# Kernel optimization log

Hardware: AMD Instinct MI355X
Metric: run time of the kernel (lower is better)

The kernel has to match this reference:

```python
import jax, jax.numpy as jnp
import numpy as np

N_NODES = 100000
N_EDGES = 1600000
D = 64          # embedding_dim (in_feats == out_feats)
H = 1           # num_heads
NEG_SLOPE = 0.2


def setup_inputs() -> dict:
    key = jax.random.key(0)
    k = jax.random.split(key, 7)
    feat = jax.random.normal(k[0], (N_NODES, D), dtype=jnp.float32)
    W = jax.random.normal(k[1], (D, H * D), dtype=jnp.float32) * (1.0 / np.sqrt(D))
    attn_l = jax.random.normal(k[2], (1, H, D), dtype=jnp.float32) * (1.0 / np.sqrt(D))
    attn_r = jax.random.normal(k[3], (1, H, D), dtype=jnp.float32) * (1.0 / np.sqrt(D))
    bias = jnp.zeros((H * D,), dtype=jnp.float32)
    src = jax.random.randint(k[4], (N_EDGES,), 0, N_NODES, dtype=jnp.int32)
    dst = jax.random.randint(k[5], (N_EDGES,), 0, N_NODES, dtype=jnp.int32)
    return {"feat": feat, "W": W, "attn_l": attn_l, "attn_r": attn_r,
            "bias": bias, "src": src, "dst": dst}


def reference(feat, W, attn_l, attn_r, bias, src, dst):
    # fc (no bias), view to [N, H, D_out]
    ft = (feat @ W).reshape(-1, H, D)                       # [N, H, D]
    # per-node attention halves
    el = jnp.sum(ft * attn_l, axis=-1, keepdims=True)       # [N, H, 1]
    er = jnp.sum(ft * attn_r, axis=-1, keepdims=True)       # [N, H, 1]
    # edge score: u_add_v then leaky_relu
    e = el[src] + er[dst]                                    # [E, H, 1]
    e = jnp.where(e > 0, e, NEG_SLOPE * e)
    # edge softmax over incoming edges of each destination node
    emax = jax.ops.segment_max(e, dst, num_segments=N_NODES)  # [N, H, 1]
    e_exp = jnp.exp(e - emax[dst])
    denom = jax.ops.segment_sum(e_exp, dst, num_segments=N_NODES)  # [N, H, 1]
    a = e_exp / denom[dst]                                   # [E, H, 1]
    # u_mul_e + sum aggregation to destination
    m = ft[src] * a                                          # [E, H, D]
    rst = jax.ops.segment_sum(m, dst, num_segments=N_NODES)  # [N, H, D]
    # residual (Identity since in_feats == out_feats) + bias
    rst = rst + feat.reshape(-1, H, D)
    rst = rst + bias.reshape(1, H, D)
    return rst
```

## Files before the change

kernel.cpp:

```cpp
#include <hip/hip_runtime.h>
#include <hip/hip_fp16.h>
#include <math.h>

#define NN 100000
#define NE 1600000
#define D 64
#define NEG_SLOPE 0.2f
#define NBKT 391
#define NBIN 391
#define CHUNKB 4096
#define BSLOT 5120
#define NTILE 1563

typedef __attribute__((ext_vector_type(8))) short short8;
typedef __attribute__((ext_vector_type(4))) float f32x4;

template<int CTRL>
__device__ __forceinline__ float dpp_add(float x) {
    int y = __builtin_amdgcn_update_dpp(0, __float_as_int(x), CTRL, 0xf, 0xf, true);
    return x + __int_as_float(y);
}
template<int CTRL>
__device__ __forceinline__ float dpp_max(float x) {
    int xi = __float_as_int(x);
    int y = __builtin_amdgcn_update_dpp(xi, xi, CTRL, 0xf, 0xf, false);
    return fmaxf(x, __int_as_float(y));
}
__device__ __forceinline__ float wave_sum63(float x) {
    x = dpp_add<0x111>(x); x = dpp_add<0x112>(x); x = dpp_add<0x114>(x);
    x = dpp_add<0x118>(x); x = dpp_add<0x142>(x); x = dpp_add<0x143>(x);
    return x;
}
__device__ __forceinline__ float wave_max63(float x) {
    x = dpp_max<0x111>(x); x = dpp_max<0x112>(x); x = dpp_max<0x114>(x);
    x = dpp_max<0x118>(x); x = dpp_max<0x142>(x); x = dpp_max<0x143>(x);
    return x;
}
__device__ __forceinline__ float rdlane_f(float v, int l) {
    return __int_as_float(__builtin_amdgcn_readlane(__float_as_int(v), l));
}
__device__ __forceinline__ unsigned bf16_1(float f) {
    unsigned x = __float_as_uint(f);
    return (x + 0x7fffu + ((x >> 16) & 1u)) >> 16;
}
__device__ __forceinline__ unsigned bfpack(float a, float b) {
    return bf16_1(a) | (bf16_1(b) << 16);
}

__global__ __launch_bounds__(256) void k_bin(const int* __restrict__ src,
                                             const int* __restrict__ dst,
                                             unsigned* __restrict__ bcnt,
                                             unsigned* __restrict__ binned) {
    __shared__ unsigned lh[NBKT];
    int t = threadIdx.x;
    unsigned b0 = blockIdx.x * CHUNKB;
    unsigned b1 = min(b0 + CHUNKB, (unsigned)NE);
    if (b0 >= b1) return;
    unsigned n4 = (b1 - b0) >> 2;
    for (int k = t; k < NBKT; k += 256) lh[k] = 0u;
    __syncthreads();
    const int4* d4 = (const int4*)(dst + b0);
    const int4* s4 = (const int4*)(src + b0);
    for (unsigned i = t; i < n4; i += 256) {
        int4 v = d4[i];
        atomicAdd(&lh[((unsigned)v.x) >> 8], 1u);
        atomicAdd(&lh[((unsigned)v.y) >> 8], 1u);
        atomicAdd(&lh[((unsigned)v.z) >> 8], 1u);
        atomicAdd(&lh[((unsigned)v.w) >> 8], 1u);
    }
    __syncthreads();
    for (int k = t; k < NBKT; k += 256) {
        unsigned c = lh[k];
        if (c) lh[k] = (unsigned)k * BSLOT + atomicAdd(&bcnt[k], c);
    }
    __syncthreads();
    for (unsigned i = t; i < n4; i += 256) {
        int4 dv = d4[i];
        int4 sv = s4[i];
        { unsigned d_=(unsigned)dv.x, s_=(unsigned)sv.x;
          unsigned pos=atomicAdd(&lh[d_>>8],1u); binned[pos]=(s_<<8)|(d_&255u); }
        { unsigned d_=(unsigned)dv.y, s_=(unsigned)sv.y;
          unsigned pos=atomicAdd(&lh[d_>>8],1u); binned[pos]=(s_<<8)|(d_&255u); }
        { unsigned d_=(unsigned)dv.z, s_=(unsigned)sv.z;
          unsigned pos=atomicAdd(&lh[d_>>8],1u); binned[pos]=(s_<<8)|(d_&255u); }
        { unsigned d_=(unsigned)dv.w, s_=(unsigned)sv.w;
          unsigned pos=atomicAdd(&lh[d_>>8],1u); binned[pos]=(s_<<8)|(d_&255u); }
    }
}

__global__ __launch_bounds__(256) void k_sg(
    const unsigned* __restrict__ bcnt, const unsigned* __restrict__ binned,
    int* __restrict__ perm, uint2* __restrict__ rowBE,
    const float* __restrict__ feat, const float* __restrict__ W,
    const float* __restrict__ attn_l, const float* __restrict__ attn_r,
    __half* __restrict__ ft, float* __restrict__ el, float* __restrict__ er)
{
    __shared__ __align__(16) char smem[22784];
    int t = threadIdx.x;

    if (blockIdx.x < NBKT) {
        unsigned* lh    = (unsigned*)smem;
        unsigned* cur   = (unsigned*)smem + 256;
        unsigned* stage = (unsigned*)smem + 512;
        int b = blockIdx.x;
        unsigned beg = (unsigned)b * BSLOT;
        unsigned cnt = min(bcnt[b], (unsigned)BSLOT);
        lh[t] = 0u;
        __syncthreads();
        for (unsigned i = t; i < cnt; i += 256) {
            unsigned w = binned[beg + i];
            stage[i] = w;
            atomicAdd(&lh[w & 255u], 1u);
        }
        __syncthreads();
        for (int off = 1; off < 256; off <<= 1) {
            unsigned u = (t >= off) ? lh[t - off] : 0u;
            __syncthreads();
            lh[t] += u;
            __syncthreads();
        }
        unsigned start = (t == 0) ? 0u : lh[t - 1];
        unsigned node = ((unsigned)b << 8) + (unsigned)t;
        if (node < NN) {
            uint2 be; be.x = beg + start; be.y = beg + lh[t];
            rowBE[node] = be;
        }
        cur[t] = start;
        __syncthreads();
        for (unsigned i = t; i < cnt; i += 256) {
            unsigned w = stage[i];
            unsigned pos = atomicAdd(&cur[w & 255u], 1u);
            perm[beg + pos] = (int)(w >> 8);
        }
        return;
    }

    unsigned short* Ab = (unsigned short*)smem;
    unsigned short* Bb = (unsigned short*)(smem + 8192);
    float* wlS = (float*)(smem + 16384);
    float* wrS = (float*)(smem + 16640);
    int n0 = (int)(blockIdx.x - NBKT) * 64;

    {
        int k = t >> 2, s = t & 3;
        float pl = 0.f, pr = 0.f;
        #pragma unroll
        for (int q = 0; q < 4; ++q) {
            int seg = s + q * 4;
            float4 f = *(const float4*)(W + k * 64 + seg * 4);
            float4 a = *(const float4*)(attn_l + seg * 4);
            float4 b = *(const float4*)(attn_r + seg * 4);
            pl += f.x*a.x + f.y*a.y + f.z*a.z + f.w*a.w;
            pr += f.x*b.x + f.y*b.y + f.z*b.z + f.w*b.w;
        }
        pl += __shfl_xor(pl, 1, 64); pl += __shfl_xor(pl, 2, 64);
        pr += __shfl_xor(pr, 1, 64); pr += __shfl_xor(pr, 2, 64);
        if (s == 0) { wlS[k] = pl; wrS[k] = pr; }
    }
    {
        int j = t & 63, g = t >> 6;
        unsigned m = (unsigned)((j & 7) << 4);
        #pragma unroll
        for (int i = 0; i < 8; ++i) {
            int k0 = g * 16 + i * 2;
            float w0 = W[k0 * 64 + j];
            float w1 = W[(k0 + 1) * 64 + j];
            *(unsigned*)((char*)Bb + j * 128 + (((unsigned)(k0 * 2)) ^ m)) = bfpack(w0, w1);
        }
    }
    __syncthreads();
    {
        int r = t >> 2, s = t & 3;
        int n = n0 + r;
        bool valid = n < NN;
        const float* fp = feat + (size_t)(valid ? n : (NN - 1)) * D;
        float pl = 0.f, pr = 0.f;
        unsigned m = (unsigned)((r & 7) << 4);
        #pragma unroll
        for (int q = 0; q < 4; ++q) {
            int seg = s + q * 4;
            float4 f = *(const float4*)(fp + seg * 4);
            float4 a = *(const float4*)(wlS + seg * 4);
            float4 b = *(const float4*)(wrS + seg * 4);
            pl += f.x*a.x + f.y*a.y + f.z*a.z + f.w*a.w;
            pr += f.x*b.x + f.y*b.y + f.z*b.z + f.w*b.w;
            uint2 pk;
            pk.x = bfpack(f.x, f.y);
            pk.y = bfpack(f.z, f.w);
            *(uint2*)((char*)Ab + r * 128 + (((unsigned)(seg * 8)) ^ m)) = pk;
        }
        pl += __shfl_xor(pl, 1, 64); pl += __shfl_xor(pl, 2, 64);
        pr += __shfl_xor(pr, 1, 64); pr += __shfl_xor(pr, 2, 64);
        if (s == 0 && valid) { el[n] = pl; er[n] = pr; }
    }
    __syncthreads();

    int w = t >> 6, l = t & 63;
    int lr = l & 15, lg = l >> 4;
    f32x4 acc0 = {0.f,0.f,0.f,0.f};
    f32x4 acc1 = {0.f,0.f,0.f,0.f};
    f32x4 acc2 = {0.f,0.f,0.f,0.f};
    f32x4 acc3 = {0.f,0.f,0.f,0.f};

    int jrow = w * 16 + lr;
    unsigned bm = (unsigned)((jrow & 7) << 4);
    short8 bf0 = *(const short8*)((char*)Bb + jrow * 128 + (((unsigned)(0 + lg * 16)) ^ bm));
    short8 bf1 = *(const short8*)((char*)Bb + jrow * 128 + (((unsigned)(64 + lg * 16)) ^ bm));

    #pragma unroll
    for (int rt = 0; rt < 4; ++rt) {
        int arow = rt * 16 + lr;
        unsigned am = (unsigned)((arow & 7) << 4);
        short8 a0 = *(const short8*)((char*)Ab + arow * 128 + (((unsigned)(0 + lg * 16)) ^ am));
        short8 a1 = *(const short8*)((char*)Ab + arow * 128 + (((unsigned)(64 + lg * 16)) ^ am));
        f32x4 acc = (rt == 0) ? acc0 : (rt == 1) ? acc1 : (rt == 2) ? acc2 : acc3;
        acc = __builtin_amdgcn_mfma_f32_16x16x32_bf16(a0, bf0, acc, 0, 0, 0);
        acc = __builtin_amdgcn_mfma_f32_16x16x32_bf16(a1, bf1, acc, 0, 0, 0);
        if (rt == 0) acc0 = acc; else if (rt == 1) acc1 = acc;
        else if (rt == 2) acc2 = acc; else acc3 = acc;
    }

    int col = w * 16 + lr;
    #pragma unroll
    for (int rt = 0; rt < 4; ++rt) {
        f32x4 acc = (rt == 0) ? acc0 : (rt == 1) ? acc1 : (rt == 2) ? acc2 : acc3;
        #pragma unroll
        for (int i = 0; i < 4; ++i) {
            int row = rt * 16 + lg * 4 + i;
            int nn = n0 + row;
            if (nn < NN) ft[(size_t)nn * D + col] = __float2half(acc[i]);
        }
    }
}

__device__ __noinline__ void agg_node64(int d, int lane, unsigned beg, unsigned end,
                                        const int* __restrict__ perm_src,
                                        const float* __restrict__ el, float er_d,
                                        const __half* __restrict__ ft,
                                        const float* __restrict__ feat,
                                        const float* __restrict__ bias,
                                        float* __restrict__ out) {
    float acc = 0.0f;
    float s = 0.0f;
    float m = -INFINITY;
    for (unsigned base = beg; base < end; base += 64) {
        unsigned i = base + lane;
        float e = -INFINITY;
        if (i < end) {
            int sid2 = perm_src[i];
            float v = el[sid2] + er_d;
            e = v > 0.0f ? v : NEG_SLOPE * v;
        }
        m = fmaxf(m, rdlane_f(wave_max63(e), 63));
    }
    for (unsigned base = beg; base < end; base += 64) {
        unsigned i = base + lane;
        float exx = 0.0f;
        if (i < end) {
            int sid2 = perm_src[i];
            float v = el[sid2] + er_d;
            v = v > 0.0f ? v : NEG_SLOPE * v;
            exx = __expf(v - m);
        }
        s += rdlane_f(wave_sum63(exx), 63);
    }
    for (unsigned jj = beg; jj < end; ++jj) {
        int sj = perm_src[jj];
        float v = el[sj] + er_d;
        v = v > 0.0f ? v : NEG_SLOPE * v;
        acc = fmaf(__half2float(ft[((size_t)sj << 6) + lane]), __expf(v - m), acc);
    }
    acc /= s;
    out[(size_t)d * D + lane] = acc + feat[(size_t)d * D + lane] + bias[lane];
}

#define LOAD8(B, J) do { \
    unsigned _o0 = (((unsigned)__builtin_amdgcn_readlane(sid, (J) + 0)) << 7) | lb; \
    unsigned _o1 = (((unsigned)__builtin_amdgcn_readlane(sid, (J) + 1)) << 7) | lb; \
    unsigned _o2 = (((unsigned)__builtin_amdgcn_readlane(sid, (J) + 2)) << 7) | lb; \
    unsigned _o3 = (((unsigned)__builtin_amdgcn_readlane(sid, (J) + 3)) << 7) | lb; \
    unsigned _o4 = (((unsigned)__builtin_amdgcn_readlane(sid, (J) + 4)) << 7) | lb; \
    unsigned _o5 = (((unsigned)__builtin_amdgcn_readlane(sid, (J) + 5)) << 7) | lb; \
    unsigned _o6 = (((unsigned)__builtin_amdgcn_readlane(sid, (J) + 6)) << 7) | lb; \
    unsigned _o7 = (((unsigned)__builtin_amdgcn_readlane(sid, (J) + 7)) << 7) | lb; \
    B##0 = *(const __half*)(ftb + _o0); \
    B##1 = *(const __half*)(ftb + _o1); \
    B##2 = *(const __half*)(ftb + _o2); \
    B##3 = *(const __half*)(ftb + _o3); \
    B##4 = *(const __half*)(ftb + _o4); \
    B##5 = *(const __half*)(ftb + _o5); \
    B##6 = *(const __half*)(ftb + _o6); \
    B##7 = *(const __half*)(ftb + _o7); \
} while (0)

#define FMA8(B, J) do { \
    acc = fmaf(__half2float(B##0), rdlane_f(ex, (J) + 0), acc); \
    acc = fmaf(__half2float(B##1), rdlane_f(ex, (J) + 1), acc); \
    acc = fmaf(__half2float(B##2), rdlane_f(ex, (J) + 2), acc); \
    acc = fmaf(__half2float(B##3), rdlane_f(ex, (J) + 3), acc); \
    acc = fmaf(__half2float(B##4), rdlane_f(ex, (J) + 4), acc); \
    acc = fmaf(__half2float(B##5), rdlane_f(ex, (J) + 5), acc); \
    acc = fmaf(__half2float(B##6), rdlane_f(ex, (J) + 6), acc); \
    acc = fmaf(__half2float(B##7), rdlane_f(ex, (J) + 7), acc); \
} while (0)

__global__ __launch_bounds__(256) void k_agg(const uint2* __restrict__ rowBE,
                                             const int* __restrict__ perm_src,
                                             const float* __restrict__ el,
                                             const float* __restrict__ er,
                                             const __half* __restrict__ ft,
                                             const float* __restrict__ feat,
                                             const float* __restrict__ bias,
                                             float* __restrict__ out) {
    int gid = blockIdx.x * 256 + threadIdx.x;
    int d = gid >> 6;
    int lane = gid & 63;
    if (d >= NN) return;

    uint2 be = rowBE[d];
    unsigned beg = be.x;
    int deg = (int)(be.y - be.x);
    float er_d = er[d];

    if (deg > 64) {
        agg_node64(d, lane, be.x, be.y, perm_src, el, er_d, ft, feat, bias, out);
        return;
    }
    if (deg == 0) {
        out[(size_t)d * D + lane] = feat[(size_t)d * D + lane] + bias[lane];
        return;
    }

    int sid = perm_src[beg + ((lane < deg) ? lane : 0)];
    float elv = el[sid];
    float fv = feat[(size_t)d * D + lane];
    float bv = bias[lane];

    const char* ftb = (const char*)ft;
    unsigned lb = (unsigned)lane << 1;

    __half c0, c1, c2, c3, c4, c5, c6, c7;
    __half n0, n1, n2, n3, n4, n5, n6, n7;
    LOAD8(c, 0);

    float e = elv + er_d;
    e = e > 0.0f ? e : NEG_SLOPE * e;
    float ex = (lane < deg) ? __expf(e) : 0.0f;
    float s = rdlane_f(wave_sum63(ex), 63);
    float inv_s = __frcp_rn(s);

    float acc = 0.0f;
    int j = 0;
    while (true) {
        bool more = (j + 8) < deg;
        if (more) LOAD8(n, j + 8);
        FMA8(c, j);
        j += 8;
        if (!more) break;
        bool more2 = (j + 8) < deg;
        if (more2) LOAD8(c, j + 8);
        FMA8(n, j);
        j += 8;
        if (!more2) break;
    }
    acc *= inv_s;
    out[(size_t)d * D + lane] = acc + fv + bv;
}

extern "C" void kernel_launch(void* const* d_in, const int* in_sizes, int n_in,
                              void* d_out, int out_size, void* d_ws, size_t ws_size,
                              hipStream_t stream) {
    const float* feat   = (const float*)d_in[0];
    const float* W      = (const float*)d_in[1];
    const float* attn_l = (const float*)d_in[2];
    const float* attn_r = (const float*)d_in[3];
    const float* bias   = (const float*)d_in[4];
    const int*   src    = (const int*)d_in[5];
    const int*   dst    = (const int*)d_in[6];
    float* out = (float*)d_out;

    char* ws = (char*)d_ws;
    __half*   ft     = (__half*)(ws);
    float*    el     = (float*)(ws + 12800000);
    float*    er     = (float*)(ws + 13200000);
    int*      perm   = (int*)(ws + 13600000);
    uint2*    rowBE  = (uint2*)(ws + 21607680);
    unsigned* bcnt   = (unsigned*)(ws + 22407680);
    unsigned* binned = (unsigned*)(ws + 22409248);

    hipMemsetAsync(bcnt, 0, NBKT * sizeof(unsigned), stream);
    k_bin<<<NBIN, 256, 0, stream>>>(src, dst, bcnt, binned);
    k_sg<<<NBKT + NTILE, 256, 0, stream>>>(bcnt, binned, perm, rowBE,
                                           feat, W, attn_l, attn_r, ft, el, er);
    k_agg<<<(NN * 64 + 255) / 256, 256, 0, stream>>>(rowBE, perm, el, er,
                                                     ft, feat, bias, out);
}
```

Baseline: 93.05 us.

## Split GEMM tiles across binning and sorting kernels to balance load

The feature GEMM tiles were all co-scheduled with the per-bucket sort in the second kernel. Now about half of them run alongside the edge-binning blocks in the first kernel and the rest stay with the sort. The aim is to fill idle CUs during the atomic-heavy binning pass and to shorten the second kernel. The GEMM body moves into a shared device function, and the first kernel's shared-memory footprint grows from the histogram alone to what the GEMM needs.

```diff
diff --git a/kernel.cpp b/kernel.cpp
--- a/kernel.cpp
+++ b/kernel.cpp
@@ -11,6 +11,7 @@
 #define CHUNKB 4096
 #define BSLOT 5120
 #define NTILE 1563
+#define NTILE_A 782
 
 typedef __attribute__((ext_vector_type(8))) short short8;
 typedef __attribute__((ext_vector_type(4))) float f32x4;
@@ -47,99 +48,17 @@
     return bf16_1(a) | (bf16_1(b) << 16);
 }
 
-__global__ __launch_bounds__(256) void k_bin(const int* __restrict__ src,
-                                             const int* __restrict__ dst,
-                                             unsigned* __restrict__ bcnt,
-                                             unsigned* __restrict__ binned) {
-    __shared__ unsigned lh[NBKT];
-    int t = threadIdx.x;
-    unsigned b0 = blockIdx.x * CHUNKB;
-    unsigned b1 = min(b0 + CHUNKB, (unsigned)NE);
-    if (b0 >= b1) return;
-    unsigned n4 = (b1 - b0) >> 2;
-    for (int k = t; k < NBKT; k += 256) lh[k] = 0u;
-    __syncthreads();
-    const int4* d4 = (const int4*)(dst + b0);
-    const int4* s4 = (const int4*)(src + b0);
-    for (unsigned i = t; i < n4; i += 256) {
-        int4 v = d4[i];
-        atomicAdd(&lh[((unsigned)v.x) >> 8], 1u);
-        atomicAdd(&lh[((unsigned)v.y) >> 8], 1u);
-        atomicAdd(&lh[((unsigned)v.z) >> 8], 1u);
-        atomicAdd(&lh[((unsigned)v.w) >> 8], 1u);
-    }
-    __syncthreads();
-    for (int k = t; k < NBKT; k += 256) {
-        unsigned c = lh[k];
-        if (c) lh[k] = (unsigned)k * BSLOT + atomicAdd(&bcnt[k], c);
-    }
-    __syncthreads();
-    for (unsigned i = t; i < n4; i += 256) {
-        int4 dv = d4[i];
-        int4 sv = s4[i];
-        { unsigned d_=(unsigned)dv.x, s_=(unsigned)sv.x;
-          unsigned pos=atomicAdd(&lh[d_>>8],1u); binned[pos]=(s_<<8)|(d_&255u); }
-        { unsigned d_=(unsigned)dv.y, s_=(unsigned)sv.y;
-          unsigned pos=atomicAdd(&lh[d_>>8],1u); binned[pos]=(s_<<8)|(d_&255u); }
-        { unsigned d_=(unsigned)dv.z, s_=(unsigned)sv.z;
-          unsigned pos=atomicAdd(&lh[d_>>8],1u); binned[pos]=(s_<<8)|(d_&255u); }
-        { unsigned d_=(unsigned)dv.w, s_=(unsigned)sv.w;
-          unsigned pos=atomicAdd(&lh[d_>>8],1u); binned[pos]=(s_<<8)|(d_&255u); }
-    }
-}
-
-__global__ __launch_bounds__(256) void k_sg(
-    const unsigned* __restrict__ bcnt, const unsigned* __restrict__ binned,
-    int* __restrict__ perm, uint2* __restrict__ rowBE,
+__device__ __forceinline__ void gemm_tile(
+    int n0, char* smem,
     const float* __restrict__ feat, const float* __restrict__ W,
     const float* __restrict__ attn_l, const float* __restrict__ attn_r,
     __half* __restrict__ ft, float* __restrict__ el, float* __restrict__ er)
 {
-    __shared__ __align__(16) char smem[22784];
-    int t = threadIdx.x;
-
-    if (blockIdx.x < NBKT) {
-        unsigned* lh    = (unsigned*)smem;
-        unsigned* cur   = (unsigned*)smem + 256;
-        unsigned* stage = (unsigned*)smem + 512;
-        int b = blockIdx.x;
-        unsigned beg = (unsigned)b * BSLOT;
-        unsigned cnt = min(bcnt[b], (unsigned)BSLOT);
-        lh[t] = 0u;
-        __syncthreads();
-        for (unsigned i = t; i < cnt; i += 256) {
-            unsigned w = binned[beg + i];
-            stage[i] = w;
-            atomicAdd(&lh[w & 255u], 1u);
-        }
-        __syncthreads();
-        for (int off = 1; off < 256; off <<= 1) {
-            unsigned u = (t >= off) ? lh[t - off] : 0u;
-            __syncthreads();
-            lh[t] += u;
-            __syncthreads();
-        }
-        unsigned start = (t == 0) ? 0u : lh[t - 1];
-        unsigned node = ((unsigned)b << 8) + (unsigned)t;
-        if (node < NN) {
-            uint2 be; be.x = beg + start; be.y = beg + lh[t];
-            rowBE[node] = be;
-        }
-        cur[t] = start;
-        __syncthreads();
-        for (unsigned i = t; i < cnt; i += 256) {
-            unsigned w = stage[i];
-            unsigned pos = atomicAdd(&cur[w & 255u], 1u);
-            perm[beg + pos] = (int)(w >> 8);
-        }
-        return;
-    }
-
     unsigned short* Ab = (unsigned short*)smem;
     unsigned short* Bb = (unsigned short*)(smem + 8192);
     float* wlS = (float*)(smem + 16384);
     float* wrS = (float*)(smem + 16640);
-    int n0 = (int)(blockIdx.x - NBKT) * 64;
+    int t = threadIdx.x;
 
     {
         int k = t >> 2, s = t & 3;
@@ -233,6 +152,107 @@
     }
 }
 
+__global__ __launch_bounds__(256) void k_bg(
+    const int* __restrict__ src, const int* __restrict__ dst,
+    unsigned* __restrict__ bcnt, unsigned* __restrict__ binned,
+    const float* __restrict__ feat, const float* __restrict__ W,
+    const float* __restrict__ attn_l, const float* __restrict__ attn_r,
+    __half* __restrict__ ft, float* __restrict__ el, float* __restrict__ er)
+{
+    __shared__ __align__(16) char smem[16896];
+    int t = threadIdx.x;
+
+    if (blockIdx.x < NBIN) {
+        unsigned* lh = (unsigned*)smem;
+        unsigned b0 = blockIdx.x * CHUNKB;
+        unsigned b1 = min(b0 + CHUNKB, (unsigned)NE);
+        if (b0 >= b1) return;
+        unsigned n4 = (b1 - b0) >> 2;
+        for (int k = t; k < NBKT; k += 256) lh[k] = 0u;
+        __syncthreads();
+        const int4* d4 = (const int4*)(dst + b0);
+        const int4* s4 = (const int4*)(src + b0);
+        for (unsigned i = t; i < n4; i += 256) {
+            int4 v = d4[i];
+            atomicAdd(&lh[((unsigned)v.x) >> 8], 1u);
+            atomicAdd(&lh[((unsigned)v.y) >> 8], 1u);
+            atomicAdd(&lh[((unsigned)v.z) >> 8], 1u);
+            atomicAdd(&lh[((unsigned)v.w) >> 8], 1u);
+        }
+        __syncthreads();
+        for (int k = t; k < NBKT; k += 256) {
+            unsigned c = lh[k];
+            if (c) lh[k] = (unsigned)k * BSLOT + atomicAdd(&bcnt[k], c);
+        }
+        __syncthreads();
+        for (unsigned i = t; i < n4; i += 256) {
+            int4 dv = d4[i];
+            int4 sv = s4[i];
+            { unsigned d_=(unsigned)dv.x, s_=(unsigned)sv.x;
+              unsigned pos=atomicAdd(&lh[d_>>8],1u); binned[pos]=(s_<<8)|(d_&255u); }
+            { unsigned d_=(unsigned)dv.y, s_=(unsigned)sv.y;
+              unsigned pos=atomicAdd(&lh[d_>>8],1u); binned[pos]=(s_<<8)|(d_&255u); }
+            { unsigned d_=(unsigned)dv.z, s_=(unsigned)sv.z;
+              unsigned pos=atomicAdd(&lh[d_>>8],1u); binned[pos]=(s_<<8)|(d_&255u); }
+            { unsigned d_=(unsigned)dv.w, s_=(unsigned)sv.w;
+              unsigned pos=atomicAdd(&lh[d_>>8],1u); binned[pos]=(s_<<8)|(d_&255u); }
+        }
+        return;
+    }
+    gemm_tile((int)(blockIdx.x - NBIN) * 64, smem,
+              feat, W, attn_l, attn_r, ft, el, er);
+}
+
+__global__ __launch_bounds__(256) void k_sg(
+    const unsigned* __restrict__ bcnt, const unsigned* __restrict__ binned,
+    int* __restrict__ perm, uint2* __restrict__ rowBE,
+    const float* __restrict__ feat, const float* __restrict__ W,
+    const float* __restrict__ attn_l, const float* __restrict__ attn_r,
+    __half* __restrict__ ft, float* __restrict__ el, float* __restrict__ er)
+{
+    __shared__ __align__(16) char smem[22784];
+    int t = threadIdx.x;
+
+    if (blockIdx.x < NBKT) {
+        unsigned* lh    = (unsigned*)smem;
+        unsigned* cur   = (unsigned*)smem + 256;
+        unsigned* stage = (unsigned*)smem + 512;
+        int b = blockIdx.x;
+        unsigned beg = (unsigned)b * BSLOT;
+        unsigned cnt = min(bcnt[b], (unsigned)BSLOT);
+        lh[t] = 0u;
+        __syncthreads();
+        for (unsigned i = t; i < cnt; i += 256) {
+            unsigned w = binned[beg + i];
+            stage[i] = w;
+            atomicAdd(&lh[w & 255u], 1u);
+        }
+        __syncthreads();
+        for (int off = 1; off < 256; off <<= 1) {
+            unsigned u = (t >= off) ? lh[t - off] : 0u;
+            __syncthreads();
+            lh[t] += u;
+            __syncthreads();
+        }
+        unsigned start = (t == 0) ? 0u : lh[t - 1];
+        unsigned node = ((unsigned)b << 8) + (unsigned)t;
+        if (node < NN) {
+            uint2 be; be.x = beg + start; be.y = beg + lh[t];
+            rowBE[node] = be;
+        }
+        cur[t] = start;
+        __syncthreads();
+        for (unsigned i = t; i < cnt; i += 256) {
+            unsigned w = stage[i];
+            unsigned pos = atomicAdd(&cur[w & 255u], 1u);
+            perm[beg + pos] = (int)(w >> 8);
+        }
+        return;
+    }
+    gemm_tile((int)(blockIdx.x - NBKT + NTILE_A) * 64, smem,
+              feat, W, attn_l, attn_r, ft, el, er);
+}
+
 __device__ __noinline__ void agg_node64(int d, int lane, unsigned beg, unsigned end,
                                         const int* __restrict__ perm_src,
                                         const float* __restrict__ el, float er_d,
@@ -389,9 +409,10 @@
     unsigned* binned = (unsigned*)(ws + 22409248);
 
     hipMemsetAsync(bcnt, 0, NBKT * sizeof(unsigned), stream);
-    k_bin<<<NBIN, 256, 0, stream>>>(src, dst, bcnt, binned);
-    k_sg<<<NBKT + NTILE, 256, 0, stream>>>(bcnt, binned, perm, rowBE,
-                                           feat, W, attn_l, attn_r, ft, el, er);
+    k_bg<<<NBIN + NTILE_A, 256, 0, stream>>>(src, dst, bcnt, binned,
+                                             feat, W, attn_l, attn_r, ft, el, er);
+    k_sg<<<NBKT + (NTILE - NTILE_A), 256, 0, stream>>>(bcnt, binned, perm, rowBE,
+                                             feat, W, attn_l, attn_r, ft, el, er);
     k_agg<<<(NN * 64 + 255) / 256, 256, 0, stream>>>(rowBE, perm, el, er,
                                                      ft, feat, bias, out);
 }
```

Result: slower. 97.38 us (+4.7%).

## Precompute per-edge exp scores during sort, move el/er to binning kernel

Applied to the files above, without the earlier changes.

Computes el/er per node in the binning kernel (extra tile blocks), so that the scatter stage can compute each edge's leaky-relu exp weight while permuting and store it in a sorted eperm array that reuses the binned buffer. The aggregation kernel then reads those precomputed weights and reads source ids from memory via scalar loads instead of readlane, and drops the max-subtraction passes for high-degree nodes. This removes repeated el gathers and exp work in aggregation, but it adds gathers into the sort stage and removes the max-stabilisation, which risks overflow on large scores.

```diff
diff --git a/kernel.cpp b/kernel.cpp
--- a/kernel.cpp
+++ b/kernel.cpp
@@ -20,22 +20,11 @@
     int y = __builtin_amdgcn_update_dpp(0, __float_as_int(x), CTRL, 0xf, 0xf, true);
     return x + __int_as_float(y);
 }
-template<int CTRL>
-__device__ __forceinline__ float dpp_max(float x) {
-    int xi = __float_as_int(x);
-    int y = __builtin_amdgcn_update_dpp(xi, xi, CTRL, 0xf, 0xf, false);
-    return fmaxf(x, __int_as_float(y));
-}
 __device__ __forceinline__ float wave_sum63(float x) {
     x = dpp_add<0x111>(x); x = dpp_add<0x112>(x); x = dpp_add<0x114>(x);
     x = dpp_add<0x118>(x); x = dpp_add<0x142>(x); x = dpp_add<0x143>(x);
     return x;
 }
-__device__ __forceinline__ float wave_max63(float x) {
-    x = dpp_max<0x111>(x); x = dpp_max<0x112>(x); x = dpp_max<0x114>(x);
-    x = dpp_max<0x118>(x); x = dpp_max<0x142>(x); x = dpp_max<0x143>(x);
-    return x;
-}
 __device__ __forceinline__ float rdlane_f(float v, int l) {
     return __int_as_float(__builtin_amdgcn_readlane(__float_as_int(v), l));
 }
@@ -47,53 +36,101 @@
     return bf16_1(a) | (bf16_1(b) << 16);
 }
 
-__global__ __launch_bounds__(256) void k_bin(const int* __restrict__ src,
-                                             const int* __restrict__ dst,
-                                             unsigned* __restrict__ bcnt,
-                                             unsigned* __restrict__ binned) {
-    __shared__ unsigned lh[NBKT];
+__global__ __launch_bounds__(256) void k_bg(
+    const int* __restrict__ src, const int* __restrict__ dst,
+    unsigned* __restrict__ bcnt, unsigned* __restrict__ binned,
+    const float* __restrict__ feat, const float* __restrict__ W,
+    const float* __restrict__ attn_l, const float* __restrict__ attn_r,
+    float* __restrict__ el, float* __restrict__ er)
+{
+    __shared__ __align__(16) char smem[1664];
     int t = threadIdx.x;
-    unsigned b0 = blockIdx.x * CHUNKB;
-    unsigned b1 = min(b0 + CHUNKB, (unsigned)NE);
-    if (b0 >= b1) return;
-    unsigned n4 = (b1 - b0) >> 2;
-    for (int k = t; k < NBKT; k += 256) lh[k] = 0u;
+
+    if (blockIdx.x < NBIN) {
+        unsigned* lh = (unsigned*)smem;
+        unsigned b0 = blockIdx.x * CHUNKB;
+        unsigned b1 = min(b0 + CHUNKB, (unsigned)NE);
+        if (b0 >= b1) return;
+        unsigned n4 = (b1 - b0) >> 2;
+        for (int k = t; k < NBKT; k += 256) lh[k] = 0u;
+        __syncthreads();
+        const int4* d4 = (const int4*)(dst + b0);
+        const int4* s4 = (const int4*)(src + b0);
+        for (unsigned i = t; i < n4; i += 256) {
+            int4 v = d4[i];
+            atomicAdd(&lh[((unsigned)v.x) >> 8], 1u);
+            atomicAdd(&lh[((unsigned)v.y) >> 8], 1u);
+            atomicAdd(&lh[((unsigned)v.z) >> 8], 1u);
+            atomicAdd(&lh[((unsigned)v.w) >> 8], 1u);
+        }
+        __syncthreads();
+        for (int k = t; k < NBKT; k += 256) {
+            unsigned c = lh[k];
+            if (c) lh[k] = (unsigned)k * BSLOT + atomicAdd(&bcnt[k], c);
+        }
+        __syncthreads();
+        for (unsigned i = t; i < n4; i += 256) {
+            int4 dv = d4[i];
+            int4 sv = s4[i];
+            { unsigned d_=(unsigned)dv.x, s_=(unsigned)sv.x;
+              unsigned pos=atomicAdd(&lh[d_>>8],1u); binned[pos]=(s_<<8)|(d_&255u); }
+            { unsigned d_=(unsigned)dv.y, s_=(unsigned)sv.y;
+              unsigned pos=atomicAdd(&lh[d_>>8],1u); binned[pos]=(s_<<8)|(d_&255u); }
+            { unsigned d_=(unsigned)dv.z, s_=(unsigned)sv.z;
+              unsigned pos=atomicAdd(&lh[d_>>8],1u); binned[pos]=(s_<<8)|(d_&255u); }
+            { unsigned d_=(unsigned)dv.w, s_=(unsigned)sv.w;
+              unsigned pos=atomicAdd(&lh[d_>>8],1u); binned[pos]=(s_<<8)|(d_&255u); }
+        }
+        return;
+    }
+
+    float* wlS = (float*)smem;
+    float* wrS = (float*)(smem + 256);
+    int n0 = (int)(blockIdx.x - NBIN) * 64;
+    {
+        int k = t >> 2, s = t & 3;
+        float pl = 0.f, pr = 0.f;
+        #pragma unroll
+        for (int q = 0; q < 4; ++q) {
+            int seg = s + q * 4;
+            float4 f = *(const float4*)(W + k * 64 + seg * 4);
+            float4 a = *(const float4*)(attn_l + seg * 4);
+            float4 b = *(const float4*)(attn_r + seg * 4);
+            pl += f.x*a.x + f.y*a.y + f.z*a.z + f.w*a.w;
+            pr += f.x*b.x + f.y*b.y + f.z*b.z + f.w*b.w;
+        }
+        pl += __shfl_xor(pl, 1, 64); pl += __shfl_xor(pl, 2, 64);
+        pr += __shfl_xor(pr, 1, 64); pr += __shfl_xor(pr, 2, 64);
+        if (s == 0) { wlS[k] = pl; wrS[k] = pr; }
+    }
     __syncthreads();
-    const int4* d4 = (const int4*)(dst + b0);
-    const int4* s4 = (const int4*)(src + b0);
-    for (unsigned i = t; i < n4; i += 256) {
-        int4 v = d4[i];
-        atomicAdd(&lh[((unsigned)v.x) >> 8], 1u);
-        atomicAdd(&lh[((unsigned)v.y) >> 8], 1u);
-        atomicAdd(&lh[((unsigned)v.z) >> 8], 1u);
-        atomicAdd(&lh[((unsigned)v.w) >> 8], 1u);
-    }
-    __syncthreads();
-    for (int k = t; k < NBKT; k += 256) {
-        unsigned c = lh[k];
-        if (c) lh[k] = (unsigned)k * BSLOT + atomicAdd(&bcnt[k], c);
-    }
-    __syncthreads();
-    for (unsigned i = t; i < n4; i += 256) {
-        int4 dv = d4[i];
-        int4 sv = s4[i];
-        { unsigned d_=(unsigned)dv.x, s_=(unsigned)sv.x;
-          unsigned pos=atomicAdd(&lh[d_>>8],1u); binned[pos]=(s_<<8)|(d_&255u); }
-        { unsigned d_=(unsigned)dv.y, s_=(unsigned)sv.y;
-          unsigned pos=atomicAdd(&lh[d_>>8],1u); binned[pos]=(s_<<8)|(d_&255u); }
-        { unsigned d_=(unsigned)dv.z, s_=(unsigned)sv.z;
-          unsigned pos=atomicAdd(&lh[d_>>8],1u); binned[pos]=(s_<<8)|(d_&255u); }
-        { unsigned d_=(unsigned)dv.w, s_=(unsigned)sv.w;
-          unsigned pos=atomicAdd(&lh[d_>>8],1u); binned[pos]=(s_<<8)|(d_&255u); }
+    {
+        int r = t >> 2, s = t & 3;
+        int n = n0 + r;
+        bool valid = n < NN;
+        const float* fp = feat + (size_t)(valid ? n : (NN - 1)) * D;
+        float pl = 0.f, pr = 0.f;
+        #pragma unroll
+        for (int q = 0; q < 4; ++q) {
+            int seg = s + q * 4;
+            float4 f = *(const float4*)(fp + seg * 4);
+            float4 a = *(const float4*)(wlS + seg * 4);
+            float4 b = *(const float4*)(wrS + seg * 4);
+            pl += f.x*a.x + f.y*a.y + f.z*a.z + f.w*a.w;
+            pr += f.x*b.x + f.y*b.y + f.z*b.z + f.w*b.w;
+        }
+        pl += __shfl_xor(pl, 1, 64); pl += __shfl_xor(pl, 2, 64);
+        pr += __shfl_xor(pr, 1, 64); pr += __shfl_xor(pr, 2, 64);
+        if (s == 0 && valid) { el[n] = pl; er[n] = pr; }
     }
 }
 
 __global__ __launch_bounds__(256) void k_sg(
     const unsigned* __restrict__ bcnt, const unsigned* __restrict__ binned,
-    int* __restrict__ perm, uint2* __restrict__ rowBE,
+    const float* __restrict__ el, const float* __restrict__ er,
+    int* __restrict__ perm, float* __restrict__ eperm, uint2* __restrict__ rowBE,
     const float* __restrict__ feat, const float* __restrict__ W,
-    const float* __restrict__ attn_l, const float* __restrict__ attn_r,
-    __half* __restrict__ ft, float* __restrict__ el, float* __restrict__ er)
+    __half* __restrict__ ft)
 {
     __shared__ __align__(16) char smem[22784];
     int t = threadIdx.x;
@@ -129,34 +166,25 @@
         __syncthreads();
         for (unsigned i = t; i < cnt; i += 256) {
             unsigned w = stage[i];
-            unsigned pos = atomicAdd(&cur[w & 255u], 1u);
-            perm[beg + pos] = (int)(w >> 8);
+            unsigned dl = w & 255u;
+            unsigned pos = atomicAdd(&cur[dl], 1u);
+            unsigned sj = w >> 8;
+            float e = el[sj] + er[((unsigned)b << 8) + dl];
+            e = e > 0.0f ? e : NEG_SLOPE * e;
+            perm[beg + pos] = (int)sj;
+            eperm[beg + pos] = __expf(e);
+        }
+        __syncthreads();
+        if (t < 8 && cnt + t < BSLOT) {
+            perm[beg + cnt + t] = 0;
+            eperm[beg + cnt + t] = 0.0f;
         }
         return;
     }
 
     unsigned short* Ab = (unsigned short*)smem;
     unsigned short* Bb = (unsigned short*)(smem + 8192);
-    float* wlS = (float*)(smem + 16384);
-    float* wrS = (float*)(smem + 16640);
     int n0 = (int)(blockIdx.x - NBKT) * 64;
-
-    {
-        int k = t >> 2, s = t & 3;
-        float pl = 0.f, pr = 0.f;
-        #pragma unroll
-        for (int q = 0; q < 4; ++q) {
-            int seg = s + q * 4;
-            float4 f = *(const float4*)(W + k * 64 + seg * 4);
-            float4 a = *(const float4*)(attn_l + seg * 4);
-            float4 b = *(const float4*)(attn_r + seg * 4);
-            pl += f.x*a.x + f.y*a.y + f.z*a.z + f.w*a.w;
-            pr += f.x*b.x + f.y*b.y + f.z*b.z + f.w*b.w;
-        }
-        pl += __shfl_xor(pl, 1, 64); pl += __shfl_xor(pl, 2, 64);
-        pr += __shfl_xor(pr, 1, 64); pr += __shfl_xor(pr, 2, 64);
-        if (s == 0) { wlS[k] = pl; wrS[k] = pr; }
-    }
     {
         int j = t & 63, g = t >> 6;
         unsigned m = (unsigned)((j & 7) << 4);
@@ -168,30 +196,21 @@
             *(unsigned*)((char*)Bb + j * 128 + (((unsigned)(k0 * 2)) ^ m)) = bfpack(w0, w1);
         }
     }
-    __syncthreads();
     {
         int r = t >> 2, s = t & 3;
         int n = n0 + r;
         bool valid = n < NN;
         const float* fp = feat + (size_t)(valid ? n : (NN - 1)) * D;
-        float pl = 0.f, pr = 0.f;
         unsigned m = (unsigned)((r & 7) << 4);
         #pragma unroll
         for (int q = 0; q < 4; ++q) {
             int seg = s + q * 4;
             float4 f = *(const float4*)(fp + seg * 4);
-            float4 a = *(const float4*)(wlS + seg * 4);
-            float4 b = *(const float4*)(wrS + seg * 4);
-            pl += f.x*a.x + f.y*a.y + f.z*a.z + f.w*a.w;
-            pr += f.x*b.x + f.y*b.y + f.z*b.z + f.w*b.w;
             uint2 pk;
             pk.x = bfpack(f.x, f.y);
             pk.y = bfpack(f.z, f.w);
             *(uint2*)((char*)Ab + r * 128 + (((unsigned)(seg * 8)) ^ m)) = pk;
         }
-        pl += __shfl_xor(pl, 1, 64); pl += __shfl_xor(pl, 2, 64);
-        pr += __shfl_xor(pr, 1, 64); pr += __shfl_xor(pr, 2, 64);
-        if (s == 0 && valid) { el[n] = pl; er[n] = pr; }
     }
     __syncthreads();
 
@@ -234,63 +253,40 @@
 }
 
 __device__ __noinline__ void agg_node64(int d, int lane, unsigned beg, unsigned end,
-                                        const int* __restrict__ perm_src,
-                                        const float* __restrict__ el, float er_d,
+                                        const int* __restrict__ perm,
+                                        const float* __restrict__ eperm,
                                         const __half* __restrict__ ft,
                                         const float* __restrict__ feat,
                                         const float* __restrict__ bias,
                                         float* __restrict__ out) {
-    float acc = 0.0f;
     float s = 0.0f;
-    float m = -INFINITY;
     for (unsigned base = beg; base < end; base += 64) {
         unsigned i = base + lane;
-        float e = -INFINITY;
-        if (i < end) {
-            int sid2 = perm_src[i];
-            float v = el[sid2] + er_d;
-            e = v > 0.0f ? v : NEG_SLOPE * v;
-        }
-        m = fmaxf(m, rdlane_f(wave_max63(e), 63));
-    }
-    for (unsigned base = beg; base < end; base += 64) {
-        unsigned i = base + lane;
-        float exx = 0.0f;
-        if (i < end) {
-            int sid2 = perm_src[i];
-            float v = el[sid2] + er_d;
-            v = v > 0.0f ? v : NEG_SLOPE * v;
-            exx = __expf(v - m);
-        }
+        float exx = (i < end) ? eperm[i] : 0.0f;
         s += rdlane_f(wave_sum63(exx), 63);
     }
+    float inv_s = __frcp_rn(s);
+    float acc = 0.0f;
     for (unsigned jj = beg; jj < end; ++jj) {
-        int sj = perm_src[jj];
-        float v = el[sj] + er_d;
-        v = v > 0.0f ? v : NEG_SLOPE * v;
-        acc = fmaf(__half2float(ft[((size_t)sj << 6) + lane]), __expf(v - m), acc);
-    }
-    acc /= s;
+        int sj = perm[jj];
+        float wj = eperm[jj];
+        acc = fmaf(__half2float(ft[((size_t)(unsigned)sj << 6) + lane]), wj, acc);
+    }
+    acc *= inv_s;
     out[(size_t)d * D + lane] = acc + feat[(size_t)d * D + lane] + bias[lane];
 }
 
 #define LOAD8(B, J) do { \
-    unsigned _o0 = (((unsigned)__builtin_amdgcn_readlane(sid, (J) + 0)) << 7) | lb; \
-    unsigned _o1 = (((unsigned)__builtin_amdgcn_readlane(sid, (J) + 1)) << 7) | lb; \
-    unsigned _o2 = (((unsigned)__builtin_amdgcn_readlane(sid, (J) + 2)) << 7) | lb; \
-    unsigned _o3 = (((unsigned)__builtin_amdgcn_readlane(sid, (J) + 3)) << 7) | lb; \
-    unsigned _o4 = (((unsigned)__builtin_amdgcn_readlane(sid, (J) + 4)) << 7) | lb; \
-    unsigned _o5 = (((unsigned)__builtin_amdgcn_readlane(sid, (J) + 5)) << 7) | lb; \
-    unsigned _o6 = (((unsigned)__builtin_amdgcn_readlane(sid, (J) + 6)) << 7) | lb; \
-    unsigned _o7 = (((unsigned)__builtin_amdgcn_readlane(sid, (J) + 7)) << 7) | lb; \
-    B##0 = *(const __half*)(ftb + _o0); \
-    B##1 = *(const __half*)(ftb + _o1); \
-    B##2 = *(const __half*)(ftb + _o2); \
-    B##3 = *(const __half*)(ftb + _o3); \
-    B##4 = *(const __half*)(ftb + _o4); \
-    B##5 = *(const __half*)(ftb + _o5); \
-    B##6 = *(const __half*)(ftb + _o6); \
-    B##7 = *(const __half*)(ftb + _o7); \
+    int _s0 = ps[(J)+0]; int _s1 = ps[(J)+1]; int _s2 = ps[(J)+2]; int _s3 = ps[(J)+3]; \
+    int _s4 = ps[(J)+4]; int _s5 = ps[(J)+5]; int _s6 = ps[(J)+6]; int _s7 = ps[(J)+7]; \
+    B##0 = *(const __half*)(ftb + (((size_t)(unsigned)_s0) << 7) + lb); \
+    B##1 = *(const __half*)(ftb + (((size_t)(unsigned)_s1) << 7) + lb); \
+    B##2 = *(const __half*)(ftb + (((size_t)(unsigned)_s2) << 7) + lb); \
+    B##3 = *(const __half*)(ftb + (((size_t)(unsigned)_s3) << 7) + lb); \
+    B##4 = *(const __half*)(ftb + (((size_t)(unsigned)_s4) << 7) + lb); \
+    B##5 = *(const __half*)(ftb + (((size_t)(unsigned)_s5) << 7) + lb); \
+    B##6 = *(const __half*)(ftb + (((size_t)(unsigned)_s6) << 7) + lb); \
+    B##7 = *(const __half*)(ftb + (((size_t)(unsigned)_s7) << 7) + lb); \
 } while (0)
 
 #define FMA8(B, J) do { \
@@ -305,9 +301,8 @@
 } while (0)
 
 __global__ __launch_bounds__(256) void k_agg(const uint2* __restrict__ rowBE,
-                                             const int* __restrict__ perm_src,
-                                             const float* __restrict__ el,
-                                             const float* __restrict__ er,
+                                             const int* __restrict__ perm,
+                                             const float* __restrict__ eperm,
                                              const __half* __restrict__ ft,
                                              const float* __restrict__ feat,
                                              const float* __restrict__ bias,
@@ -320,10 +315,9 @@
     uint2 be = rowBE[d];
     unsigned beg = be.x;
     int deg = (int)(be.y - be.x);
-    float er_d = er[d];
 
     if (deg > 64) {
-        agg_node64(d, lane, be.x, be.y, perm_src, el, er_d, ft, feat, bias, out);
+        agg_node64(d, lane, be.x, be.y, perm, eperm, ft, feat, bias, out);
         return;
     }
     if (deg == 0) {
@@ -331,33 +325,32 @@
         return;
     }
 
-    int sid = perm_src[beg + ((lane < deg) ? lane : 0)];
-    float elv = el[sid];
+    float ex = (lane < deg) ? eperm[beg + lane] : 0.0f;
     float fv = feat[(size_t)d * D + lane];
     float bv = bias[lane];
 
+    unsigned begu = __builtin_amdgcn_readfirstlane(beg);
+    int degu = __builtin_amdgcn_readfirstlane(deg);
+    const int* ps = perm + begu;
     const char* ftb = (const char*)ft;
-    unsigned lb = (unsigned)lane << 1;
+    size_t lb = (size_t)((unsigned)lane << 1);
 
     __half c0, c1, c2, c3, c4, c5, c6, c7;
     __half n0, n1, n2, n3, n4, n5, n6, n7;
     LOAD8(c, 0);
 
-    float e = elv + er_d;
-    e = e > 0.0f ? e : NEG_SLOPE * e;
-    float ex = (lane < deg) ? __expf(e) : 0.0f;
     float s = rdlane_f(wave_sum63(ex), 63);
     float inv_s = __frcp_rn(s);
 
     float acc = 0.0f;
     int j = 0;
     while (true) {
-        bool more = (j + 8) < deg;
+        bool more = (j + 8) < degu;
         if (more) LOAD8(n, j + 8);
         FMA8(c, j);
         j += 8;
         if (!more) break;
-        bool more2 = (j + 8) < deg;
+        bool more2 = (j + 8) < degu;
         if (more2) LOAD8(c, j + 8);
         FMA8(n, j);
         j += 8;
@@ -387,11 +380,13 @@
     uint2*    rowBE  = (uint2*)(ws + 21607680);
     unsigned* bcnt   = (unsigned*)(ws + 22407680);
     unsigned* binned = (unsigned*)(ws + 22409248);
+    float*    eperm  = (float*)binned;
 
     hipMemsetAsync(bcnt, 0, NBKT * sizeof(unsigned), stream);
-    k_bin<<<NBIN, 256, 0, stream>>>(src, dst, bcnt, binned);
-    k_sg<<<NBKT + NTILE, 256, 0, stream>>>(bcnt, binned, perm, rowBE,
-                                           feat, W, attn_l, attn_r, ft, el, er);
-    k_agg<<<(NN * 64 + 255) / 256, 256, 0, stream>>>(rowBE, perm, el, er,
+    k_bg<<<NBIN + NTILE, 256, 0, stream>>>(src, dst, bcnt, binned,
+                                           feat, W, attn_l, attn_r, el, er);
+    k_sg<<<NBKT + NTILE, 256, 0, stream>>>(bcnt, binned, el, er,
+                                           perm, eperm, rowBE, feat, W, ft);
+    k_agg<<<(NN * 64 + 255) / 256, 256, 0, stream>>>(rowBE, perm, eperm,
                                                      ft, feat, bias, out);
 }
```

New measurement: 102.9 us. 1.11x slower.
